# Kernel tuning notes

Measured on AMD Instinct MI355X. Metric: run time of the kernel, lower is better.

Reference implementation:

```python
import jax, jax.numpy as jnp
import numpy as np

B, VH, VL, EP = 4, 130, 120, 256
DIN, DEP, D, H, NL = 256, 128, 512, 16, 8
HID = 4 * D

def _pe(x, base=1000.0):
    # sinusoidal positional encoding (base=1000 as in the module)
    L, Dm = x.shape[-2], x.shape[-1]
    pos = jnp.arange(L, dtype=jnp.float32)
    ch = jnp.arange(Dm, dtype=jnp.float32)
    ang = pos[:, None] / (base ** (2.0 * ch / ch[-1]))[None]
    enc = jnp.where(ch % 2 == 0, jnp.sin(ang), jnp.cos(ang))
    return x + enc

def _ln(x, g, b):
    m = x.mean(-1, keepdims=True)
    v = ((x - m) ** 2).mean(-1, keepdims=True)
    return (x - m) / jnp.sqrt(v + 1e-5) * g + b

def _gmha(x, rots, trans, mask_bias, qkv_w, out_w, out_b, g, b, r_s, d_s):
    # ESM3 geometric multi-head attention (algorithm 6)
    xn = _ln(x, g, b)
    qkv = (xn @ qkv_w.T).reshape(x.shape[0], x.shape[1], 5, H, 3)  # [B,L,5,H,3]
    qkv = jnp.einsum('brid,brfhd->brfhi', rots, qkv)               # rotate into global frame
    Qr, Kr, Qd, Kd, V = (qkv[..., f, :, :] for f in range(5))
    scale = 3.0 ** -0.5
    Ar = jnp.einsum('bihd,bjhd->bijh', Qr, Kr) * jax.nn.softplus(r_s) * scale
    qd = Qd + trans[:, :, None, :]
    kd = Kd + trans[:, :, None, :]
    dist = jnp.linalg.norm(qd[:, :, None] - kd[:, None], axis=-1)  # [B,i,j,H]
    logits = Ar - dist * jax.nn.softplus(d_s) * scale + mask_bias[..., None]
    A = jax.nn.softmax(logits, axis=2)
    o = jnp.einsum('bijh,bjhd->bihd', A, V)
    o = jnp.einsum('brji,brhj->brhi', rots, o)                     # rotate back (R^T)
    return o.reshape(x.shape[0], x.shape[1], H * 3) @ out_w.T + out_b

def _swiglu(x, g, b, w12, w3):
    # SwiGLU transition (dropout is identity in eval)
    h = _ln(x, g, b) @ w12.T
    a, v = jnp.split(h, 2, axis=-1)
    return (jax.nn.silu(a) * v) @ w3.T

def _forward(vh_x, vl_x, vh_rots, vh_trans, vl_rots, vl_trans, ep_feats, ep_rots, ep_trans,
             vh_emb_w, vl_emb_w, tgt_emb_w, qkv_w, out_w, out_b, ln_g, ln_b, r_scale, d_scale,
             ln2_g, ln2_b, w12, w3, out_vh_w, out_vh_gate_w, out_vh_gate_b,
             out_vl_w, out_vl_gate_w, out_vl_gate_b, vh_mask, vl_mask, ep_mask):
    emb = jnp.concatenate([_pe(vh_x @ vh_emb_w.T), _pe(vl_x @ vl_emb_w.T), ep_feats @ tgt_emb_w.T], axis=1)
    rots = jnp.concatenate([vh_rots, vl_rots, ep_rots], axis=1)
    trans = jnp.concatenate([vh_trans, vl_trans, ep_trans], axis=1)
    mask = jnp.concatenate([vh_mask, vl_mask, ep_mask], axis=1)
    mask_bias = jnp.where(mask[:, :, None] | mask[:, None, :], -1e9, 0.0)
    for i in range(NL):
        emb = emb + _gmha(emb, rots, trans, mask_bias, qkv_w[i], out_w[i], out_b[i],
                          ln_g[i], ln_b[i], r_scale[i], d_scale[i])
        emb = emb + _swiglu(emb, ln2_g[i], ln2_b[i], w12[i], w3[i])
    vh_e, vl_e = emb[:, :VH], emb[:, VH:VH + VL]
    vh_upd = (vh_e @ out_vh_w.T) * jax.nn.sigmoid(vh_e @ out_vh_gate_w.T + out_vh_gate_b)
    vl_upd = (vl_e @ out_vl_w.T) * jax.nn.sigmoid(vl_e @ out_vl_gate_w.T + out_vl_gate_b)
    vh_out = jnp.where(~vh_mask[..., None], vh_x + vh_upd, vh_x)
    vl_out = jnp.where(~vl_mask[..., None], vl_x + vl_upd, vl_x)
    return vh_out, vl_out

def setup_inputs():
    key = jax.random.key(0)
    ks = iter(jax.random.split(key, 40))
    s = 0.02
    return dict(
        vh_x=jax.random.normal(next(ks), (B, VH, DIN)),
        vl_x=jax.random.normal(next(ks), (B, VL, DIN)),
        vh_rots=jax.random.normal(next(ks), (B, VH, 3, 3)),
        vh_trans=jax.random.normal(next(ks), (B, VH, 3)),
        vl_rots=jax.random.normal(next(ks), (B, VL, 3, 3)),
        vl_trans=jax.random.normal(next(ks), (B, VL, 3)),
        ep_feats=jax.random.normal(next(ks), (B, EP, DEP)),
        ep_rots=jax.random.normal(next(ks), (B, EP, 3, 3)),
        ep_trans=jax.random.normal(next(ks), (B, EP, 3)),
        vh_mask=jnp.zeros((B, VH), dtype=bool),
        vl_mask=jnp.zeros((B, VL), dtype=bool),
        ep_mask=jax.random.randint(next(ks), (B, EP), 0, 2).astype(bool),
        vh_emb_w=jax.random.normal(next(ks), (D, DIN)) * s,
        vl_emb_w=jax.random.normal(next(ks), (D, DIN)) * s,
        tgt_emb_w=jax.random.normal(next(ks), (D, DEP)) * s,
        qkv_w=jax.random.normal(next(ks), (NL, H * 15, D)) * s,
        out_w=jax.random.normal(next(ks), (NL, D, H * 3)) * s,
        out_b=jnp.zeros((NL, D)),
        ln_g=jnp.ones((NL, D)), ln_b=jnp.zeros((NL, D)),
        r_scale=jnp.zeros((NL, H)), d_scale=jnp.zeros((NL, H)),
        ln2_g=jnp.ones((NL, D)), ln2_b=jnp.zeros((NL, D)),
        w12=jax.random.normal(next(ks), (NL, 2 * HID, D)) * s,
        w3=jax.random.normal(next(ks), (NL, D, HID)) * s,
        out_vh_w=jax.random.normal(next(ks), (DIN, D)) * s,
        out_vh_gate_w=jax.random.normal(next(ks), (DIN, D)) * s,
        out_vh_gate_b=jnp.full((DIN,), -2.0),
        out_vl_w=jax.random.normal(next(ks), (DIN, D)) * s,
        out_vl_gate_w=jax.random.normal(next(ks), (DIN, D)) * s,
        out_vl_gate_b=jnp.full((DIN,), -2.0),
    )

def reference(vh_x, vl_x, vh_rots, vh_trans, vl_rots, vl_trans, ep_feats, ep_rots, ep_trans,
              vh_mask, vl_mask, ep_mask,
              vh_emb_w, vl_emb_w, tgt_emb_w, qkv_w, out_w, out_b, ln_g, ln_b, r_scale, d_scale,
              ln2_g, ln2_b, w12, w3, out_vh_w, out_vh_gate_w, out_vh_gate_b,
              out_vl_w, out_vl_gate_w, out_vl_gate_b):
    return _forward(vh_x, vl_x, vh_rots, vh_trans, vl_rots, vl_trans, ep_feats, ep_rots, ep_trans,
                    vh_emb_w, vl_emb_w, tgt_emb_w, qkv_w, out_w, out_b, ln_g, ln_b, r_scale, d_scale,
                    ln2_g, ln2_b, w12, w3, out_vh_w, out_vh_gate_w, out_vh_gate_b,
                    out_vl_w, out_vl_gate_w, out_vl_gate_b, vh_mask, vl_mask, ep_mask)
```

## Files before the change

### kernel.cpp

```cpp
#include <hip/hip_runtime.h>
#include <hip/hip_bf16.h>
#include <math.h>
#include <stdint.h>

#define B_ 4
#define VH_ 130
#define VL_ 120
#define EP_ 256
#define R_ 506
#define RP_ 512
#define DIN_ 256
#define DEP_ 128
#define D_ 512
#define H_ 16
#define NL_ 8
#define HID_ 2048

#define MODE_STORE 0
#define MODE_ADD_BIAS 1

typedef _Float16 half8 __attribute__((ext_vector_type(8)));
typedef float f32x4 __attribute__((ext_vector_type(4)));

#define ASYNC16(ldsdst, gsrc)                                                  \
  __builtin_amdgcn_global_load_lds(                                            \
      (const __attribute__((address_space(1))) unsigned int*)(gsrc),           \
      (__attribute__((address_space(3))) unsigned int*)(ldsdst), 16, 0, 0)

__global__ __launch_bounds__(256) void gemm16_kernel(
    const _Float16* __restrict__ A, const _Float16* __restrict__ W,
    float* __restrict__ C, const float* __restrict__ bias,
    int M, int N, int K, int mode) {
  __shared__ _Float16 Al[4][4096];
  __shared__ _Float16 Bl[4][2048];

  const int t = threadIdx.x;
  const int nbm = (M + 127) >> 7;
  const int nwg = gridDim.x;
  int bid = blockIdx.x;
  if ((nwg & 7) == 0) {
    int q = nwg >> 3;
    bid = (bid & 7) * q + (bid >> 3);
  }
  const int bm = bid % nbm, bn = bid / nbm;
  const int lane = t & 63;
  const int w = t >> 6;
  const int wm = w >> 1, wn = w & 1;

  const int r0 = t >> 2;
  const int cp = t & 3;
  const int gc = cp ^ ((r0 >> 1) & 3);
  int gr0 = bm * 128 + r0;       if (gr0 >= M) gr0 = M - 1;
  int gr1 = bm * 128 + 64 + r0;  if (gr1 >= M) gr1 = M - 1;
  int gcol = bn * 64 + r0;       if (gcol >= N) gcol = N - 1;
  const _Float16* pA0 = A + (size_t)gr0 * K + gc * 8;
  const _Float16* pA1 = A + (size_t)gr1 * K + gc * 8;
  const _Float16* pB  = W + (size_t)gcol * K + gc * 8;

#define STAGE(buf, kt)                                                         \
  do {                                                                         \
    ASYNC16(&Al[buf][t * 8], pA0 + (size_t)(kt) * 32);                         \
    ASYNC16(&Al[buf][2048 + t * 8], pA1 + (size_t)(kt) * 32);                  \
    ASYNC16(&Bl[buf][t * 8], pB + (size_t)(kt) * 32);                          \
  } while (0)

  f32x4 acc[4][2];
#pragma unroll
  for (int i = 0; i < 4; i++)
#pragma unroll
    for (int j = 0; j < 2; j++) acc[i][j] = (f32x4){0.f, 0.f, 0.f, 0.f};

  const int nt = K >> 5;
  STAGE(0, 0); STAGE(1, 1); STAGE(2, 2);

  const int rl = lane & 15;
  const int ca = (lane >> 4) ^ ((rl >> 1) & 3);
  for (int kt = 0; kt < nt; ++kt) {
    if (kt < nt - 2)       asm volatile("s_waitcnt vmcnt(6)" ::: "memory");
    else if (kt == nt - 2) asm volatile("s_waitcnt vmcnt(3)" ::: "memory");
    else                   asm volatile("s_waitcnt vmcnt(0)" ::: "memory");
    __builtin_amdgcn_s_barrier();
    const int buf = kt & 3;
    const _Float16* Ab = &Al[buf][(wm * 64 + rl) * 32 + ca * 8];
    const _Float16* Bb = &Bl[buf][(wn * 32 + rl) * 32 + ca * 8];
    half8 af[4], bf[2];
#pragma unroll
    for (int i = 0; i < 4; i++) af[i] = *(const half8*)(Ab + i * 512);
#pragma unroll
    for (int j = 0; j < 2; j++) bf[j] = *(const half8*)(Bb + j * 512);
#pragma unroll
    for (int i = 0; i < 4; i++)
#pragma unroll
      for (int j = 0; j < 2; j++)
        acc[i][j] = __builtin_amdgcn_mfma_f32_16x16x32_f16(af[i], bf[j],
                                                           acc[i][j], 0, 0, 0);
    if (kt + 3 < nt) STAGE((kt + 3) & 3, kt + 3);
  }
#undef STAGE

  const int rb = bm * 128 + wm * 64 + ((lane >> 4) << 2);
  const int cb = bn * 64 + wn * 32 + (lane & 15);
#pragma unroll
  for (int i = 0; i < 4; i++) {
#pragma unroll
    for (int j = 0; j < 2; j++) {
      int col = cb + j * 16;
      if (col >= N) continue;
#pragma unroll
      for (int q = 0; q < 4; q++) {
        int row = rb + i * 16 + q;
        if (row >= M) continue;
        size_t idx = (size_t)row * N + col;
        float v = acc[i][j][q];
        if (mode == MODE_STORE) C[idx] = v;
        else {
          float bb = bias ? bias[col] : 0.f;
          C[idx] = C[idx] + v + bb;
        }
      }
    }
  }
}

__global__ __launch_bounds__(256) void gemm16sw_kernel(
    const _Float16* __restrict__ A, const _Float16* __restrict__ Wa,
    const _Float16* __restrict__ Wv, _Float16* __restrict__ Gh,
    int M, int K) {
  __shared__ _Float16 Al[4][4096];
  __shared__ _Float16 Ba[4][2048];
  __shared__ _Float16 Bv[4][2048];

  const int t = threadIdx.x;
  const int nbm = (M + 127) >> 7;
  const int nwg = gridDim.x;
  int bid = blockIdx.x;
  if ((nwg & 7) == 0) {
    int q = nwg >> 3;
    bid = (bid & 7) * q + (bid >> 3);
// ... 73 lines not shown
#pragma unroll
    for (int j = 0; j < 2; j++) {
      int col = cb + j * 16;
#pragma unroll
      for (int q = 0; q < 4; q++) {
        int row = rb + i * 16 + q;
        if (row >= M) continue;
        float a = aca[i][j][q];
        float v = acv[i][j][q];
        Gh[(size_t)row * HID_ + col] = (_Float16)((a / (1.f + expf(-a))) * v);
      }
    }
  }
}

__global__ __launch_bounds__(256) void gemm_kernel(
    const float* __restrict__ A, const float* __restrict__ W,
    float* __restrict__ C, const float* __restrict__ bias,
    int M, int N, int K,
    int A_rpb, int A_R, int A_base,
    int C_rpb, int C_R, int C_base,
    int mode) {
  __shared__ __align__(16) float As[16][68];
  __shared__ __align__(16) float Bs[16][68];

  const int t = threadIdx.x;
  const int bm = blockIdx.y, bn = blockIdx.x;
  const int ty = t >> 4, tx = t & 15;
  const int lr = t >> 2;
  const int c0 = (t & 3) * 4;

  const int ma = bm * 64 + lr;
  const bool va = (ma < M);
  int ar = 0;
  if (va) ar = (ma / A_rpb) * A_R + A_base + (ma % A_rpb);
  const float* pA = A + (size_t)ar * K + c0;

  const int nw = bn * 64 + lr;
  const bool vw = (nw < N);
  const float* pW = W + (size_t)nw * K + c0;

  float acc[4][4];
#pragma unroll
  for (int i = 0; i < 4; i++)
#pragma unroll
    for (int j = 0; j < 4; j++) acc[i][j] = 0.f;

  for (int k0 = 0; k0 < K; k0 += 16) {
    __syncthreads();
    float4 avv = va ? *(const float4*)(pA + k0) : make_float4(0.f, 0.f, 0.f, 0.f);
    float4 wvv = vw ? *(const float4*)(pW + k0) : make_float4(0.f, 0.f, 0.f, 0.f);
    As[c0 + 0][lr] = avv.x; As[c0 + 1][lr] = avv.y;
    As[c0 + 2][lr] = avv.z; As[c0 + 3][lr] = avv.w;
    Bs[c0 + 0][lr] = wvv.x; Bs[c0 + 1][lr] = wvv.y;
    Bs[c0 + 2][lr] = wvv.z; Bs[c0 + 3][lr] = wvv.w;
    __syncthreads();
#pragma unroll
    for (int kk = 0; kk < 16; kk++) {
      float4 a = *(const float4*)&As[kk][ty * 4];
      float4 bv = *(const float4*)&Bs[kk][tx * 4];
      float av[4] = {a.x, a.y, a.z, a.w};
      float bb[4] = {bv.x, bv.y, bv.z, bv.w};
#pragma unroll
      for (int i = 0; i < 4; i++)
#pragma unroll
        for (int j = 0; j < 4; j++) acc[i][j] += av[i] * bb[j];
    }
  }

  const int m0 = bm * 64 + ty * 4;
  const int n0 = bn * 64 + tx * 4;
#pragma unroll
  for (int i = 0; i < 4; i++) {
    int m = m0 + i;
    if (m >= M) continue;
    int crow = (m / C_rpb) * C_R + C_base + (m % C_rpb);
    float* cp = C + (size_t)crow * N;
#pragma unroll
    for (int j = 0; j < 4; j++) {
      int n = n0 + j;
      if (n >= N) continue;
      float r = acc[i][j];
      if (mode == MODE_STORE) cp[n] = r;
      else { float bb = bias ? bias[n] : 0.f; cp[n] = cp[n] + r + bb; }
    }
  }
}

__global__ __launch_bounds__(256) void ln_kernel(
    const float* __restrict__ x, const float* __restrict__ g,
    const float* __restrict__ b, _Float16* __restrict__ out) {
  const int row = blockIdx.x;
  const int t = threadIdx.x;
  const float* xr = x + (size_t)row * D_;
  float v0 = xr[t], v1 = xr[t + 256];
  float s = v0 + v1, s2 = v0 * v0 + v1 * v1;
#pragma unroll
  for (int o = 32; o > 0; o >>= 1) {
    s += __shfl_down(s, o);
// ... 6 lines not shown
  if (t == 0) {
    float ss = w1[0] + w1[1] + w1[2] + w1[3];
    float ss2 = w2[0] + w2[1] + w2[2] + w2[3];
    float mean = ss * (1.f / D_);
    float var = ss2 * (1.f / D_) - mean * mean;
    mv[0] = mean;
    mv[1] = rsqrtf(var + 1e-5f);
  }
  __syncthreads();
  float mean = mv[0], inv = mv[1];
  _Float16* orow = out + (size_t)row * D_;
  orow[t] = (_Float16)((v0 - mean) * inv * g[t] + b[t]);
  orow[t + 256] = (_Float16)((v1 - mean) * inv * g[t + 256] + b[t + 256]);
}

__global__ void tohalf_kernel(const float* __restrict__ src,
                              _Float16* __restrict__ dst, int n8) {
  for (int i = blockIdx.x * blockDim.x + threadIdx.x; i < n8;
       i += gridDim.x * blockDim.x) {
    const float4* s = (const float4*)(src + (size_t)i * 8);
    float4 x = s[0], y = s[1];
    half8 h = {(_Float16)x.x, (_Float16)x.y, (_Float16)x.z, (_Float16)x.w,
               (_Float16)y.x, (_Float16)y.y, (_Float16)y.z, (_Float16)y.w};
    *(half8*)(dst + (size_t)i * 8) = h;
  }
}

__global__ void concat_kernel(
    const float* __restrict__ vh_rots, const float* __restrict__ vh_trans,
    const float* __restrict__ vl_rots, const float* __restrict__ vl_trans,
    const float* __restrict__ ep_rots, const float* __restrict__ ep_trans,
    const int* __restrict__ vh_mask, const int* __restrict__ vl_mask,
    const int* __restrict__ ep_mask,
    float* __restrict__ rots, float* __restrict__ trans, int* __restrict__ mask) {
  int idx = blockIdx.x * blockDim.x + threadIdx.x;
  if (idx >= B_ * R_) return;
  int b = idx / R_, r = idx % R_;
  const float* sr; const float* st; int sm;
  if (r < VH_) {
    sr = vh_rots + (size_t)(b * VH_ + r) * 9;
    st = vh_trans + (size_t)(b * VH_ + r) * 3;
    sm = vh_mask[b * VH_ + r];
  } else if (r < VH_ + VL_) {
    int rr = r - VH_;
    sr = vl_rots + (size_t)(b * VL_ + rr) * 9;
    st = vl_trans + (size_t)(b * VL_ + rr) * 3;
    sm = vl_mask[b * VL_ + rr];
  } else {
    int rr = r - VH_ - VL_;
    sr = ep_rots + (size_t)(b * EP_ + rr) * 9;
    st = ep_trans + (size_t)(b * EP_ + rr) * 3;
    sm = ep_mask[b * EP_ + rr];
  }
#pragma unroll
  for (int k = 0; k < 9; k++) rots[(size_t)idx * 9 + k] = sr[k];
#pragma unroll
  for (int k = 0; k < 3; k++) trans[(size_t)idx * 3 + k] = st[k];
  mask[idx] = sm;
}

__global__ void pad_kernel(const int* __restrict__ mask_c, int* __restrict__ maskp,
                           float* __restrict__ Kt, float* __restrict__ PKt,
                           float* __restrict__ Vt) {
  int idx = blockIdx.x * blockDim.x + threadIdx.x;
  if (idx < B_ * RP_) {
    int b = idx >> 9, j = idx & (RP_ - 1);
    maskp[idx] = (j < R_) ? mask_c[b * R_ + j] : 1;
  } else if (idx < B_ * RP_ + 3 * B_ * H_ * 3 * (RP_ - R_)) {
    int p = idx - B_ * RP_;
    int a = p / (B_ * H_ * 3 * (RP_ - R_));
    int q = p % (B_ * H_ * 3 * (RP_ - R_));
    int chan = q / (RP_ - R_), jj = q % (RP_ - R_);
    float* dst = (a == 0) ? Kt : (a == 1) ? PKt : Vt;
    dst[(size_t)chan * RP_ + R_ + jj] = 0.f;
  }
}

__global__ void pe_kernel(float* __restrict__ emb) {
  int idx = blockIdx.x * blockDim.x + threadIdx.x;
  const int total = B_ * (VH_ + VL_) * D_;
  if (idx >= total) return;
  int d = idx & (D_ - 1);
  int rb = idx >> 9;
  int r = rb % (VH_ + VL_);
  int b = rb / (VH_ + VL_);
  float pos = (r < VH_) ? (float)r : (float)(r - VH_);
  float ang = pos * expf((float)d * (-2.0f / 511.0f) * 6.907755278982137f);
  float enc = (d & 1) ? cosf(ang) : sinf(ang);
  emb[((size_t)b * R_ + r) * D_ + d] += enc;
}

__global__ __launch_bounds__(128) void rotate_kernel(
    const float* __restrict__ qkv_raw, const float* __restrict__ rots,
    const float* __restrict__ trans, float* __restrict__ Qrow,
    float* __restrict__ PQrow, float* __restrict__ Kt,
    float* __restrict__ PKt, float* __restrict__ Vt) {
  const int blk = blockIdx.x;
  const int b = blk / R_;
  const int r = blk % R_;
  const int t = threadIdx.x;
  __shared__ float Rm[9], tr[3], raw[240];
  if (t < 9) Rm[t] = rots[(size_t)blk * 9 + t];
  if (t >= 9 && t < 12) tr[t - 9] = trans[(size_t)blk * 3 + (t - 9)];
  for (int i = t; i < 240; i += 128) raw[i] = qkv_raw[(size_t)blk * 240 + i];
// ... 13 lines not shown
      dst[o] = r0; dst[o + 1] = r1; dst[o + 2] = r2;
    } else {
      float* dst = (f == 1) ? Kt : (f == 3) ? PKt : Vt;
      size_t base = ((size_t)(b * H_ + h) * 3) * RP_ + r;
      dst[base] = r0; dst[base + RP_] = r1; dst[base + 2 * RP_] = r2;
    }
  }
}

__global__ __launch_bounds__(256) void attn2_kernel(
    const float* __restrict__ Qrow, const float* __restrict__ PQrow,
    const float* __restrict__ Kt, const float* __restrict__ PKt,
    const float* __restrict__ Vt, const float* __restrict__ rots,
    const int* __restrict__ mask, const int* __restrict__ maskp,
    const float* __restrict__ rs, const float* __restrict__ ds,
    float* __restrict__ o) {
  const int blk = blockIdx.x;
  const int b = blk / (R_ / 2);
  const int ip = blk % (R_ / 2);
  const int i0 = ip * 2;
  const int t = threadIdx.x;
  const int lane = t & 63;
  const int w = t >> 6;

  __shared__ float qs[2][48], ps[2][48], og[2][48];
  __shared__ float crs[16], cds[16];
  __shared__ int mi[2];

  if (t < 96) {
    int io = t / 48, k2 = t % 48;
    int i = i0 + io;
// ... 62 lines not shown
      ox0 += p0 * vx; oy0 += p0 * vy; oz0 += p0 * vz;
      ox1 += p1 * vx; oy1 += p1 * vy; oz1 += p1 * vz;
    }
#pragma unroll
    for (int s = 1; s < 64; s <<= 1) {
      s0 += __shfl_xor(s0, s); s1 += __shfl_xor(s1, s);
      ox0 += __shfl_xor(ox0, s); oy0 += __shfl_xor(oy0, s); oz0 += __shfl_xor(oz0, s);
      ox1 += __shfl_xor(ox1, s); oy1 += __shfl_xor(oy1, s); oz1 += __shfl_xor(oz1, s);
    }
    if (lane == 0) {
      og[0][h * 3] = ox0 / s0; og[0][h * 3 + 1] = oy0 / s0; og[0][h * 3 + 2] = oz0 / s0;
      og[1][h * 3] = ox1 / s1; og[1][h * 3 + 1] = oy1 / s1; og[1][h * 3 + 2] = oz1 / s1;
    }
  }
  __syncthreads();
  if (t < 96) {
    int io = t / 48, idx = t % 48;
    int h = idx / 3, i3 = idx % 3;
    int i = i0 + io;
    const float* Rm = rots + ((size_t)(b * R_ + i)) * 9;
    float val = Rm[0 + i3] * og[io][h * 3 + 0] +
                Rm[3 + i3] * og[io][h * 3 + 1] +
                Rm[6 + i3] * og[io][h * 3 + 2];
    o[((size_t)(b * R_ + i)) * 48 + idx] = val;
  }
}

__global__ void combine_kernel(
    const float* __restrict__ x, const float* __restrict__ t1,
    const float* __restrict__ t2, const float* __restrict__ gate_b,
    const int* __restrict__ mask, float* __restrict__ out, int total) {
  int idx = blockIdx.x * blockDim.x + threadIdx.x;
  if (idx >= total) return;
  int dm = idx & (DIN_ - 1);
  int row = idx >> 8;
  float xv = x[idx];
  if (mask[row]) {
    out[idx] = xv;
  } else {
    float gate = 1.f / (1.f + expf(-(t2[idx] + gate_b[dm])));
    out[idx] = xv + t1[idx] * gate;
  }
}

extern "C" void kernel_launch(void* const* d_in, const int* in_sizes, int n_in,
                              void* d_out, int out_size, void* d_ws, size_t ws_size,
                              hipStream_t stream) {
  const float* vh_x = (const float*)d_in[0];
  const float* vl_x = (const float*)d_in[1];
  const float* vh_rots = (const float*)d_in[2];
  const float* vh_trans = (const float*)d_in[3];
  const float* vl_rots = (const float*)d_in[4];
  const float* vl_trans = (const float*)d_in[5];
  const float* ep_feats = (const float*)d_in[6];
  const float* ep_rots = (const float*)d_in[7];
  const float* ep_trans = (const float*)d_in[8];
// ... 22 lines not shown
  const float* out_vl_gate_b = (const float*)d_in[31];

  const int BR = B_ * R_;

  uint8_t* P = (uint8_t*)d_ws;
  auto alloc = [&](size_t bytes) {
    uint8_t* p = P;
    P += (bytes + 255) & ~(size_t)255;
    return p;
  };
  float* emb = (float*)alloc((size_t)BR * D_ * 4);
  _Float16* xnh = (_Float16*)alloc((size_t)BR * D_ * 2);
  float* qkvr = (float*)alloc((size_t)BR * 240 * 4);
  float* Qrow = (float*)alloc((size_t)BR * 48 * 4);
  float* PQrow = (float*)alloc((size_t)BR * 48 * 4);
  float* ob = (float*)alloc((size_t)BR * 48 * 4);
  float* Kt = (float*)alloc((size_t)B_ * H_ * 3 * RP_ * 4);
  float* PKt = (float*)alloc((size_t)B_ * H_ * 3 * RP_ * 4);
  float* Vt = (float*)alloc((size_t)B_ * H_ * 3 * RP_ * 4);
  _Float16* ghalf = (_Float16*)alloc((size_t)BR * HID_ * 2);
  float* rots_c = (float*)alloc((size_t)BR * 9 * 4);
  float* trans_c = (float*)alloc((size_t)BR * 3 * 4);
  int* mask_c = (int*)alloc((size_t)BR * 4);
  int* maskp = (int*)alloc((size_t)B_ * RP_ * 4);
  float* t1 = (float*)alloc((size_t)B_ * VH_ * DIN_ * 4);
  float* t2 = (float*)alloc((size_t)B_ * VH_ * DIN_ * 4);
  _Float16* qkvh = (_Float16*)alloc((size_t)NL_ * 240 * D_ * 2);
  _Float16* w12h = (_Float16*)alloc((size_t)NL_ * 2 * HID_ * D_ * 2);
  _Float16* w3h = (_Float16*)alloc((size_t)NL_ * D_ * HID_ * 2);

  auto gemm32 = [&](const float* A, const float* W, float* C, const float* bias,
                    int M, int N, int K, int Arpb, int AR, int Abase, int Crpb,
                    int CR, int Cbase, int mode) {
    dim3 g((N + 63) / 64, (M + 63) / 64);
    gemm_kernel<<<g, 256, 0, stream>>>(A, W, C, bias, M, N, K, Arpb, AR, Abase,
                                       Crpb, CR, Cbase, mode);
  };
  auto gemm16 = [&](const _Float16* A, const _Float16* W, float* C,
                    const float* bias, int M, int N, int K, int mode) {
    int nbm = (M + 127) / 128, nbn = (N + 63) / 64;
    gemm16_kernel<<<nbm * nbn, 256, 0, stream>>>(A, W, C, bias, M, N, K, mode);
  };

  {
    int n8q = NL_ * 240 * D_ / 8;
    int n8a = NL_ * 2 * HID_ * D_ / 8;
    int n8c = NL_ * D_ * HID_ / 8;
    tohalf_kernel<<<dim3(min((n8q + 255) / 256, 2048)), 256, 0, stream>>>(qkv_w, qkvh, n8q);
    tohalf_kernel<<<dim3(min((n8a + 255) / 256, 4096)), 256, 0, stream>>>(w12, w12h, n8a);
    tohalf_kernel<<<dim3(min((n8c + 255) / 256, 4096)), 256, 0, stream>>>(w3, w3h, n8c);
  }

  concat_kernel<<<(BR + 255) / 256, 256, 0, stream>>>(
      vh_rots, vh_trans, vl_rots, vl_trans, ep_rots, ep_trans, vh_mask,
      vl_mask, ep_mask, rots_c, trans_c, mask_c);
  {
    int total = B_ * RP_ + 3 * B_ * H_ * 3 * (RP_ - R_);
    pad_kernel<<<(total + 255) / 256, 256, 0, stream>>>(mask_c, maskp, Kt, PKt, Vt);
  }

  gemm32(vh_x, vh_emb_w, emb, nullptr, B_ * VH_, D_, DIN_, B_ * VH_, B_ * VH_, 0,
         VH_, R_, 0, MODE_STORE);
  gemm32(vl_x, vl_emb_w, emb, nullptr, B_ * VL_, D_, DIN_, B_ * VL_, B_ * VL_, 0,
         VL_, R_, VH_, MODE_STORE);
  gemm32(ep_feats, tgt_emb_w, emb, nullptr, B_ * EP_, D_, DEP_, B_ * EP_,
         B_ * EP_, 0, EP_, R_, VH_ + VL_, MODE_STORE);
  {
    int total = B_ * (VH_ + VL_) * D_;
    pe_kernel<<<(total + 255) / 256, 256, 0, stream>>>(emb);
  }

  for (int l = 0; l < NL_; l++) {
    const _Float16* qwh = qkvh + (size_t)l * 240 * D_;
    const float* ow = out_w + (size_t)l * D_ * 48;
    const float* obias = out_b + (size_t)l * D_;
    const float* lg = ln_g + (size_t)l * D_;
    const float* lb = ln_b + (size_t)l * D_;
    const float* l2g = ln2_g + (size_t)l * D_;
    const float* l2b = ln2_b + (size_t)l * D_;
    const float* rs = r_scale + (size_t)l * H_;
    const float* dsc = d_scale + (size_t)l * H_;
    const _Float16* w12ah = w12h + (size_t)l * 2 * HID_ * D_;
    const _Float16* w12bh = w12ah + (size_t)HID_ * D_;
    const _Float16* w3lh = w3h + (size_t)l * D_ * HID_;

    ln_kernel<<<BR, 256, 0, stream>>>(emb, lg, lb, xnh);
    gemm16(xnh, qwh, qkvr, nullptr, BR, 240, D_, MODE_STORE);
    rotate_kernel<<<BR, 128, 0, stream>>>(qkvr, rots_c, trans_c, Qrow, PQrow,
                                          Kt, PKt, Vt);
    attn2_kernel<<<B_ * (R_ / 2), 256, 0, stream>>>(Qrow, PQrow, Kt, PKt, Vt,
                                                    rots_c, mask_c, maskp, rs,
                                                    dsc, ob);
    gemm32(ob, ow, emb, obias, BR, D_, 48, BR, BR, 0, BR, BR, 0, MODE_ADD_BIAS);

    ln_kernel<<<BR, 256, 0, stream>>>(emb, l2g, l2b, xnh);
    {
      int nbm = (BR + 127) / 128, nbn = HID_ / 64;
      gemm16sw_kernel<<<nbm * nbn, 256, 0, stream>>>(xnh, w12ah, w12bh, ghalf,
                                                     BR, D_);
    }
    gemm16(ghalf, w3lh, emb, nullptr, BR, D_, HID_, MODE_ADD_BIAS);
  }

  gemm32(emb, out_vh_w, t1, nullptr, B_ * VH_, DIN_, D_, VH_, R_, 0, B_ * VH_,
         B_ * VH_, 0, MODE_STORE);
  gemm32(emb, out_vh_gate_w, t2, nullptr, B_ * VH_, DIN_, D_, VH_, R_, 0,
         B_ * VH_, B_ * VH_, 0, MODE_STORE);
  {
    int total = B_ * VH_ * DIN_;
    combine_kernel<<<(total + 255) / 256, 256, 0, stream>>>(
        vh_x, t1, t2, out_vh_gate_b, vh_mask, (float*)d_out, total);
  }
  gemm32(emb, out_vl_w, t1, nullptr, B_ * VL_, DIN_, D_, VL_, R_, VH_, B_ * VL_,
         B_ * VL_, 0, MODE_STORE);
  gemm32(emb, out_vl_gate_w, t2, nullptr, B_ * VL_, DIN_, D_, VL_, R_, VH_,
         B_ * VL_, B_ * VL_, 0, MODE_STORE);
  {
    int total = B_ * VL_ * DIN_;
    combine_kernel<<<(total + 255) / 256, 256, 0, stream>>>(
        vl_x, t1, t2, out_vl_gate_b, vl_mask,
        (float*)d_out + (size_t)B_ * VH_ * DIN_, total);
  }
}
```

Baseline: 1.324 ms.

## Replace fp32 GEMMs with fp16 MFMA, fuse PE, out-proj, gating, prep kernels

```diff
diff --git a/kernel.cpp b/kernel.cpp
--- a/kernel.cpp
+++ b/kernel.cpp
@@ -27,101 +27,6 @@
       (const __attribute__((address_space(1))) unsigned int*)(gsrc),           \
       (__attribute__((address_space(3))) unsigned int*)(ldsdst), 16, 0, 0)
 
-__global__ __launch_bounds__(256) void gemm16_kernel(
-    const _Float16* __restrict__ A, const _Float16* __restrict__ W,
-    float* __restrict__ C, const float* __restrict__ bias,
-    int M, int N, int K, int mode) {
-  __shared__ _Float16 Al[4][4096];
-  __shared__ _Float16 Bl[4][2048];
-
-  const int t = threadIdx.x;
-  const int nbm = (M + 127) >> 7;
-  const int nwg = gridDim.x;
-  int bid = blockIdx.x;
-  if ((nwg & 7) == 0) {
-    int q = nwg >> 3;
-    bid = (bid & 7) * q + (bid >> 3);
-  }
-  const int bm = bid % nbm, bn = bid / nbm;
-  const int lane = t & 63;
-  const int w = t >> 6;
-  const int wm = w >> 1, wn = w & 1;
-
-  const int r0 = t >> 2;
-  const int cp = t & 3;
-  const int gc = cp ^ ((r0 >> 1) & 3);
-  int gr0 = bm * 128 + r0;       if (gr0 >= M) gr0 = M - 1;
-  int gr1 = bm * 128 + 64 + r0;  if (gr1 >= M) gr1 = M - 1;
-  int gcol = bn * 64 + r0;       if (gcol >= N) gcol = N - 1;
-  const _Float16* pA0 = A + (size_t)gr0 * K + gc * 8;
-  const _Float16* pA1 = A + (size_t)gr1 * K + gc * 8;
-  const _Float16* pB  = W + (size_t)gcol * K + gc * 8;
-
-#define STAGE(buf, kt)                                                         \
-  do {                                                                         \
-    ASYNC16(&Al[buf][t * 8], pA0 + (size_t)(kt) * 32);                         \
-    ASYNC16(&Al[buf][2048 + t * 8], pA1 + (size_t)(kt) * 32);                  \
-    ASYNC16(&Bl[buf][t * 8], pB + (size_t)(kt) * 32);                          \
-  } while (0)
-
-  f32x4 acc[4][2];
-#pragma unroll
-  for (int i = 0; i < 4; i++)
-#pragma unroll
-    for (int j = 0; j < 2; j++) acc[i][j] = (f32x4){0.f, 0.f, 0.f, 0.f};
-
-  const int nt = K >> 5;
-  STAGE(0, 0); STAGE(1, 1); STAGE(2, 2);
-
-  const int rl = lane & 15;
-  const int ca = (lane >> 4) ^ ((rl >> 1) & 3);
-  for (int kt = 0; kt < nt; ++kt) {
-    if (kt < nt - 2)       asm volatile("s_waitcnt vmcnt(6)" ::: "memory");
-    else if (kt == nt - 2) asm volatile("s_waitcnt vmcnt(3)" ::: "memory");
-    else                   asm volatile("s_waitcnt vmcnt(0)" ::: "memory");
-    __builtin_amdgcn_s_barrier();
-    const int buf = kt & 3;
-    const _Float16* Ab = &Al[buf][(wm * 64 + rl) * 32 + ca * 8];
-    const _Float16* Bb = &Bl[buf][(wn * 32 + rl) * 32 + ca * 8];
-    half8 af[4], bf[2];
-#pragma unroll
-    for (int i = 0; i < 4; i++) af[i] = *(const half8*)(Ab + i * 512);
-#pragma unroll
-    for (int j = 0; j < 2; j++) bf[j] = *(const half8*)(Bb + j * 512);
-#pragma unroll
-    for (int i = 0; i < 4; i++)
-#pragma unroll
-      for (int j = 0; j < 2; j++)
-        acc[i][j] = __builtin_amdgcn_mfma_f32_16x16x32_f16(af[i], bf[j],
-                                                           acc[i][j], 0, 0, 0);
-    if (kt + 3 < nt) STAGE((kt + 3) & 3, kt + 3);
-  }
-#undef STAGE
-
-  const int rb = bm * 128 + wm * 64 + ((lane >> 4) << 2);
-  const int cb = bn * 64 + wn * 32 + (lane & 15);
-#pragma unroll
-  for (int i = 0; i < 4; i++) {
-#pragma unroll
-    for (int j = 0; j < 2; j++) {
-      int col = cb + j * 16;
-      if (col >= N) continue;
-#pragma unroll
-      for (int q = 0; q < 4; q++) {
-        int row = rb + i * 16 + q;
-        if (row >= M) continue;
-        size_t idx = (size_t)row * N + col;
-        float v = acc[i][j][q];
-        if (mode == MODE_STORE) C[idx] = v;
-        else {
-          float bb = bias ? bias[col] : 0.f;
-          C[idx] = C[idx] + v + bb;
-        }
-      }
-    }
-  }
-}
-
 __global__ __launch_bounds__(256) void gemm16sw_kernel(
     const _Float16* __restrict__ A, const _Float16* __restrict__ Wa,
     const _Float16* __restrict__ Wv, _Float16* __restrict__ Gh,
@@ -225,75 +130,208 @@
   }
 }
 
-__global__ __launch_bounds__(256) void gemm_kernel(
-    const float* __restrict__ A, const float* __restrict__ W,
+__global__ __launch_bounds__(256) void gemm16b_kernel(
+    const _Float16* __restrict__ A, const _Float16* __restrict__ W,
     float* __restrict__ C, const float* __restrict__ bias,
-    int M, int N, int K,
-    int A_rpb, int A_R, int A_base,
-    int C_rpb, int C_R, int C_base,
-    int mode) {
-  __shared__ __align__(16) float As[16][68];
-  __shared__ __align__(16) float Bs[16][68];
+    int M, int N, int K, int mode, int crpb, int cR, int cbase, int pe) {
+  __shared__ _Float16 Al[4][2048];
+  __shared__ _Float16 Bl[4][2048];
 
   const int t = threadIdx.x;
-  const int bm = blockIdx.y, bn = blockIdx.x;
-  const int ty = t >> 4, tx = t & 15;
-  const int lr = t >> 2;
-  const int c0 = (t & 3) * 4;
-
-  const int ma = bm * 64 + lr;
-  const bool va = (ma < M);
-  int ar = 0;
-  if (va) ar = (ma / A_rpb) * A_R + A_base + (ma % A_rpb);
-  const float* pA = A + (size_t)ar * K + c0;
-
-  const int nw = bn * 64 + lr;
-  const bool vw = (nw < N);
-  const float* pW = W + (size_t)nw * K + c0;
-
-  float acc[4][4];
-#pragma unroll
-  for (int i = 0; i < 4; i++)
-#pragma unroll
-    for (int j = 0; j < 4; j++) acc[i][j] = 0.f;
-
-  for (int k0 = 0; k0 < K; k0 += 16) {
-    __syncthreads();
-    float4 avv = va ? *(const float4*)(pA + k0) : make_float4(0.f, 0.f, 0.f, 0.f);
-    float4 wvv = vw ? *(const float4*)(pW + k0) : make_float4(0.f, 0.f, 0.f, 0.f);
-    As[c0 + 0][lr] = avv.x; As[c0 + 1][lr] = avv.y;
-    As[c0 + 2][lr] = avv.z; As[c0 + 3][lr] = avv.w;
-    Bs[c0 + 0][lr] = wvv.x; Bs[c0 + 1][lr] = wvv.y;
-    Bs[c0 + 2][lr] = wvv.z; Bs[c0 + 3][lr] = wvv.w;
-    __syncthreads();
-#pragma unroll
-    for (int kk = 0; kk < 16; kk++) {
-      float4 a = *(const float4*)&As[kk][ty * 4];
-      float4 bv = *(const float4*)&Bs[kk][tx * 4];
-      float av[4] = {a.x, a.y, a.z, a.w};
-      float bb[4] = {bv.x, bv.y, bv.z, bv.w};
-#pragma unroll
-      for (int i = 0; i < 4; i++)
-#pragma unroll
-        for (int j = 0; j < 4; j++) acc[i][j] += av[i] * bb[j];
-    }
-  }
-
-  const int m0 = bm * 64 + ty * 4;
-  const int n0 = bn * 64 + tx * 4;
-#pragma unroll
-  for (int i = 0; i < 4; i++) {
-    int m = m0 + i;
-    if (m >= M) continue;
-    int crow = (m / C_rpb) * C_R + C_base + (m % C_rpb);
-    float* cp = C + (size_t)crow * N;
-#pragma unroll
-    for (int j = 0; j < 4; j++) {
-      int n = n0 + j;
-      if (n >= N) continue;
-      float r = acc[i][j];
-      if (mode == MODE_STORE) cp[n] = r;
-      else { float bb = bias ? bias[n] : 0.f; cp[n] = cp[n] + r + bb; }
+  const int nbm = (M + 63) >> 6;
+  const int nwg = gridDim.x;
+  int bid = blockIdx.x;
+  if ((nwg & 7) == 0) {
+    int q = nwg >> 3;
+    bid = (bid & 7) * q + (bid >> 3);
+  }
+  const int bm = bid % nbm, bn = bid / nbm;
+  const int lane = t & 63;
+  const int w = t >> 6;
+  const int wm = w >> 1, wn = w & 1;
+
+  const int r0 = t >> 2;
+  const int cp = t & 3;
+  const int gc = cp ^ ((r0 >> 1) & 3);
+  int gr = bm * 64 + r0;    if (gr >= M) gr = M - 1;
+  int gcol = bn * 64 + r0;  if (gcol >= N) gcol = N - 1;
+  const _Float16* pA = A + (size_t)gr * K + gc * 8;
+  const _Float16* pB = W + (size_t)gcol * K + gc * 8;
+
+#define STAGE(buf, kt)                                                         \
+  do {                                                                         \
+    ASYNC16(&Al[buf][t * 8], pA + (size_t)(kt) * 32);                          \
+    ASYNC16(&Bl[buf][t * 8], pB + (size_t)(kt) * 32);                          \
+  } while (0)
+
+  f32x4 acc[2][2];
+#pragma unroll
+  for (int i = 0; i < 2; i++)
+#pragma unroll
+    for (int j = 0; j < 2; j++) acc[i][j] = (f32x4){0.f, 0.f, 0.f, 0.f};
+
+  const int nt = K >> 5;
+  STAGE(0, 0); STAGE(1, 1); STAGE(2, 2);
+
+  const int rl = lane & 15;
+  const int ca = (lane >> 4) ^ ((rl >> 1) & 3);
+  for (int kt = 0; kt < nt; ++kt) {
+    if (kt < nt - 2)       asm volatile("s_waitcnt vmcnt(4)" ::: "memory");
+    else if (kt == nt - 2) asm volatile("s_waitcnt vmcnt(2)" ::: "memory");
+    else                   asm volatile("s_waitcnt vmcnt(0)" ::: "memory");
+    __builtin_amdgcn_s_barrier();
+    const int buf = kt & 3;
+    half8 af[2], bf[2];
+#pragma unroll
+    for (int i = 0; i < 2; i++)
+      af[i] = *(const half8*)&Al[buf][(wm * 32 + i * 16 + rl) * 32 + ca * 8];
+#pragma unroll
+    for (int j = 0; j < 2; j++)
+      bf[j] = *(const half8*)&Bl[buf][(wn * 32 + j * 16 + rl) * 32 + ca * 8];
+#pragma unroll
+    for (int i = 0; i < 2; i++)
+#pragma unroll
+      for (int j = 0; j < 2; j++)
+        acc[i][j] = __builtin_amdgcn_mfma_f32_16x16x32_f16(af[i], bf[j],
+                                                           acc[i][j], 0, 0, 0);
+    if (kt + 3 < nt) STAGE((kt + 3) & 3, kt + 3);
+  }
+#undef STAGE
+
+  const float PEK = -0.02703623196464017f;
+  const int rb = bm * 64 + wm * 32 + ((lane >> 4) << 2);
+  const int cb = bn * 64 + wn * 32 + (lane & 15);
+#pragma unroll
+  for (int i = 0; i < 2; i++) {
+#pragma unroll
+    for (int j = 0; j < 2; j++) {
+      int col = cb + j * 16;
+      if (col >= N) continue;
+#pragma unroll
+      for (int q = 0; q < 4; q++) {
+        int row = rb + i * 16 + q;
+        if (row >= M) continue;
+        int crow = (row / crpb) * cR + cbase + row % crpb;
+        size_t idx = (size_t)crow * N + col;
+        float v = acc[i][j][q];
+        if (pe) {
+          float pos = (float)(row % crpb);
+          float ang = pos * expf((float)col * PEK);
+          v += (col & 1) ? cosf(ang) : sinf(ang);
+        }
+        if (mode == MODE_STORE) C[idx] = v;
+        else {
+          float bb = bias ? bias[col] : 0.f;
+          C[idx] = C[idx] + v + bb;
+        }
+      }
+    }
+  }
+}
+
+__global__ __launch_bounds__(256) void gemm16gate_kernel(
+    const _Float16* __restrict__ A, const _Float16* __restrict__ Wv,
+    const _Float16* __restrict__ Wg, const float* __restrict__ x,
+    const float* __restrict__ gb, const int* __restrict__ mask,
+    float* __restrict__ out, int M, int K, int arpb, int aR, int abase) {
+  __shared__ _Float16 Al[4][2048];
+  __shared__ _Float16 Bva[4][2048];
+  __shared__ _Float16 Bga[4][2048];
+
+  const int t = threadIdx.x;
+  const int nbm = (M + 63) >> 6;
+  const int nwg = gridDim.x;
+  int bid = blockIdx.x;
+  if ((nwg & 7) == 0) {
+    int q = nwg >> 3;
+    bid = (bid & 7) * q + (bid >> 3);
+  }
+  const int bm = bid % nbm, bn = bid / nbm;
+  const int lane = t & 63;
+  const int w = t >> 6;
+  const int wm = w >> 1, wn = w & 1;
+
+  const int r0 = t >> 2;
+  const int cp = t & 3;
+  const int gc = cp ^ ((r0 >> 1) & 3);
+  int gr = bm * 64 + r0;  if (gr >= M) gr = M - 1;
+  int ar = (gr / arpb) * aR + abase + gr % arpb;
+  const int gcol = bn * 64 + r0;
+  const _Float16* pA  = A + (size_t)ar * K + gc * 8;
+  const _Float16* pBv = Wv + (size_t)gcol * K + gc * 8;
+  const _Float16* pBg = Wg + (size_t)gcol * K + gc * 8;
+
+#define STAGE(buf, kt)                                                         \
+  do {                                                                         \
+    ASYNC16(&Al[buf][t * 8], pA + (size_t)(kt) * 32);                          \
+    ASYNC16(&Bva[buf][t * 8], pBv + (size_t)(kt) * 32);                        \
+    ASYNC16(&Bga[buf][t * 8], pBg + (size_t)(kt) * 32);                        \
+  } while (0)
+
+  f32x4 acv[2][2], acg[2][2];
+#pragma unroll
+  for (int i = 0; i < 2; i++)
+#pragma unroll
+    for (int j = 0; j < 2; j++) {
+      acv[i][j] = (f32x4){0.f, 0.f, 0.f, 0.f};
+      acg[i][j] = (f32x4){0.f, 0.f, 0.f, 0.f};
+    }
+
+  const int nt = K >> 5;
+  STAGE(0, 0); STAGE(1, 1); STAGE(2, 2);
+
+  const int rl = lane & 15;
+  const int ca = (lane >> 4) ^ ((rl >> 1) & 3);
+  for (int kt = 0; kt < nt; ++kt) {
+    if (kt < nt - 2)       asm volatile("s_waitcnt vmcnt(6)" ::: "memory");
+    else if (kt == nt - 2) asm volatile("s_waitcnt vmcnt(3)" ::: "memory");
+    else                   asm volatile("s_waitcnt vmcnt(0)" ::: "memory");
+    __builtin_amdgcn_s_barrier();
+    const int buf = kt & 3;
+    half8 af[2], bv[2], bg2[2];
+#pragma unroll
+    for (int i = 0; i < 2; i++)
+      af[i] = *(const half8*)&Al[buf][(wm * 32 + i * 16 + rl) * 32 + ca * 8];
+#pragma unroll
+    for (int j = 0; j < 2; j++) {
+      bv[j] = *(const half8*)&Bva[buf][(wn * 32 + j * 16 + rl) * 32 + ca * 8];
+      bg2[j] = *(const half8*)&Bga[buf][(wn * 32 + j * 16 + rl) * 32 + ca * 8];
+    }
+#pragma unroll
+    for (int i = 0; i < 2; i++)
+#pragma unroll
+      for (int j = 0; j < 2; j++) {
+        acv[i][j] = __builtin_amdgcn_mfma_f32_16x16x32_f16(af[i], bv[j],
+                                                           acv[i][j], 0, 0, 0);
+        acg[i][j] = __builtin_amdgcn_mfma_f32_16x16x32_f16(af[i], bg2[j],
+                                                           acg[i][j], 0, 0, 0);
+      }
+    if (kt + 3 < nt) STAGE((kt + 3) & 3, kt + 3);
+  }
+#undef STAGE
+
+  const int rb = bm * 64 + wm * 32 + ((lane >> 4) << 2);
+  const int cb = bn * 64 + wn * 32 + (lane & 15);
+#pragma unroll
+  for (int i = 0; i < 2; i++) {
+#pragma unroll
+    for (int j = 0; j < 2; j++) {
+      int col = cb + j * 16;
+#pragma unroll
+      for (int q = 0; q < 4; q++) {
+        int row = rb + i * 16 + q;
+        if (row >= M) continue;
+        size_t idx = (size_t)row * DIN_ + col;
+        float xv = x[idx];
+        float res;
+        if (mask[row]) {
+          res = xv;
+        } else {
+          float gate = 1.f / (1.f + expf(-(acg[i][j][q] + gb[col])));
+          res = xv + acv[i][j][q] * gate;
+        }
+        out[idx] = res;
+      }
     }
   }
 }
@@ -330,6 +368,26 @@
   orow[t + 256] = (_Float16)((v1 - mean) * inv * g[t + 256] + b[t + 256]);
 }
 
+struct ThSegs {
+  const float* src[13];
+  _Float16* dst[13];
+  int cum[14];
+};
+__global__ void tohalf_multi_kernel(ThSegs sg) {
+  int total = sg.cum[13];
+  for (int i = blockIdx.x * blockDim.x + threadIdx.x; i < total;
+       i += gridDim.x * blockDim.x) {
+    int s = 0;
+    while (i >= sg.cum[s + 1]) s++;
+    int off = i - sg.cum[s];
+    const float4* p = (const float4*)(sg.src[s] + (size_t)off * 8);
+    float4 x = p[0], y = p[1];
+    half8 h = {(_Float16)x.x, (_Float16)x.y, (_Float16)x.z, (_Float16)x.w,
+               (_Float16)y.x, (_Float16)y.y, (_Float16)y.z, (_Float16)y.w};
+    *(half8*)(sg.dst[s] + (size_t)off * 8) = h;
+  }
+}
+
 __global__ void tohalf_kernel(const float* __restrict__ src,
                               _Float16* __restrict__ dst, int n8) {
   for (int i = blockIdx.x * blockDim.x + threadIdx.x; i < n8;
@@ -342,68 +400,55 @@
   }
 }
 
-__global__ void concat_kernel(
+__global__ void prep_kernel(
     const float* __restrict__ vh_rots, const float* __restrict__ vh_trans,
     const float* __restrict__ vl_rots, const float* __restrict__ vl_trans,
     const float* __restrict__ ep_rots, const float* __restrict__ ep_trans,
     const int* __restrict__ vh_mask, const int* __restrict__ vl_mask,
-    const int* __restrict__ ep_mask,
-    float* __restrict__ rots, float* __restrict__ trans, int* __restrict__ mask) {
-  int idx = blockIdx.x * blockDim.x + threadIdx.x;
-  if (idx >= B_ * R_) return;
-  int b = idx / R_, r = idx % R_;
-  const float* sr; const float* st; int sm;
-  if (r < VH_) {
-    sr = vh_rots + (size_t)(b * VH_ + r) * 9;
-    st = vh_trans + (size_t)(b * VH_ + r) * 3;
-    sm = vh_mask[b * VH_ + r];
-  } else if (r < VH_ + VL_) {
-    int rr = r - VH_;
-    sr = vl_rots + (size_t)(b * VL_ + rr) * 9;
-    st = vl_trans + (size_t)(b * VL_ + rr) * 3;
-    sm = vl_mask[b * VL_ + rr];
-  } else {
-    int rr = r - VH_ - VL_;
-    sr = ep_rots + (size_t)(b * EP_ + rr) * 9;
-    st = ep_trans + (size_t)(b * EP_ + rr) * 3;
-    sm = ep_mask[b * EP_ + rr];
-  }
-#pragma unroll
-  for (int k = 0; k < 9; k++) rots[(size_t)idx * 9 + k] = sr[k];
-#pragma unroll
-  for (int k = 0; k < 3; k++) trans[(size_t)idx * 3 + k] = st[k];
-  mask[idx] = sm;
-}
-
-__global__ void pad_kernel(const int* __restrict__ mask_c, int* __restrict__ maskp,
-                           float* __restrict__ Kt, float* __restrict__ PKt,
-                           float* __restrict__ Vt) {
+    const int* __restrict__ ep_mask, float* __restrict__ rots,
+    float* __restrict__ trans, int* __restrict__ mask,
+    int* __restrict__ maskp, float* __restrict__ Kt, float* __restrict__ PKt,
+    float* __restrict__ Vt) {
   int idx = blockIdx.x * blockDim.x + threadIdx.x;
   if (idx < B_ * RP_) {
-    int b = idx >> 9, j = idx & (RP_ - 1);
-    maskp[idx] = (j < R_) ? mask_c[b * R_ + j] : 1;
-  } else if (idx < B_ * RP_ + 3 * B_ * H_ * 3 * (RP_ - R_)) {
+    int b = idx >> 9, r = idx & (RP_ - 1);
+    if (r >= R_) {
+      maskp[idx] = 1;
+      return;
+    }
+    const float* sr; const float* st; int sm;
+    if (r < VH_) {
+      sr = vh_rots + (size_t)(b * VH_ + r) * 9;
+      st = vh_trans + (size_t)(b * VH_ + r) * 3;
+      sm = vh_mask[b * VH_ + r];
+    } else if (r < VH_ + VL_) {
+      int rr = r - VH_;
+      sr = vl_rots + (size_t)(b * VL_ + rr) * 9;
+      st = vl_trans + (size_t)(b * VL_ + rr) * 3;
+      sm = vl_mask[b * VL_ + rr];
+    } else {
+      int rr = r - VH_ - VL_;
+      sr = ep_rots + (size_t)(b * EP_ + rr) * 9;
+      st = ep_trans + (size_t)(b * EP_ + rr) * 3;
+      sm = ep_mask[b * EP_ + rr];
+    }
+    int lin = b * R_ + r;
+    maskp[idx] = sm;
+    mask[lin] = sm;
+#pragma unroll
+    for (int k = 0; k < 9; k++) rots[(size_t)lin * 9 + k] = sr[k];
+#pragma unroll
+    for (int k = 0; k < 3; k++) trans[(size_t)lin * 3 + k] = st[k];
+  } else {
     int p = idx - B_ * RP_;
-    int a = p / (B_ * H_ * 3 * (RP_ - R_));
-    int q = p % (B_ * H_ * 3 * (RP_ - R_));
+    const int per = B_ * H_ * 3 * (RP_ - R_);
+    if (p >= 3 * per) return;
+    int a = p / per;
+    int q = p % per;
     int chan = q / (RP_ - R_), jj = q % (RP_ - R_);
     float* dst = (a == 0) ? Kt : (a == 1) ? PKt : Vt;
     dst[(size_t)chan * RP_ + R_ + jj] = 0.f;
   }
-}
-
-__global__ void pe_kernel(float* __restrict__ emb) {
-  int idx = blockIdx.x * blockDim.x + threadIdx.x;
-  const int total = B_ * (VH_ + VL_) * D_;
-  if (idx >= total) return;
-  int d = idx & (D_ - 1);
-  int rb = idx >> 9;
-  int r = rb % (VH_ + VL_);
-  int b = rb / (VH_ + VL_);
-  float pos = (r < VH_) ? (float)r : (float)(r - VH_);
-  float ang = pos * expf((float)d * (-2.0f / 511.0f) * 6.907755278982137f);
-  float enc = (d & 1) ? cosf(ang) : sinf(ang);
-  emb[((size_t)b * R_ + r) * D_ + d] += enc;
 }
 
 __global__ __launch_bounds__(128) void rotate_kernel(
@@ -447,7 +492,8 @@
     const float* __restrict__ Vt, const float* __restrict__ rots,
     const int* __restrict__ mask, const int* __restrict__ maskp,
     const float* __restrict__ rs, const float* __restrict__ ds,
-    float* __restrict__ o) {
+    const float* __restrict__ out_w, const float* __restrict__ out_b,
+    float* __restrict__ emb) {
   const int blk = blockIdx.x;
   const int b = blk / (R_ / 2);
   const int ip = blk % (R_ / 2);
@@ -540,32 +586,31 @@
     }
   }
   __syncthreads();
-  if (t < 96) {
-    int io = t / 48, idx = t % 48;
-    int h = idx / 3, i3 = idx % 3;
-    int i = i0 + io;
-    const float* Rm = rots + ((size_t)(b * R_ + i)) * 9;
-    float val = Rm[0 + i3] * og[io][h * 3 + 0] +
-                Rm[3 + i3] * og[io][h * 3 + 1] +
-                Rm[6 + i3] * og[io][h * 3 + 2];
-    o[((size_t)(b * R_ + i)) * 48 + idx] = val;
-  }
-}
-
-__global__ void combine_kernel(
-    const float* __restrict__ x, const float* __restrict__ t1,
-    const float* __restrict__ t2, const float* __restrict__ gate_b,
-    const int* __restrict__ mask, float* __restrict__ out, int total) {
-  int idx = blockIdx.x * blockDim.x + threadIdx.x;
-  if (idx >= total) return;
-  int dm = idx & (DIN_ - 1);
-  int row = idx >> 8;
-  float xv = x[idx];
-  if (mask[row]) {
-    out[idx] = xv;
-  } else {
-    float gate = 1.f / (1.f + expf(-(t2[idx] + gate_b[dm])));
-    out[idx] = xv + t1[idx] * gate;
+  float r0v0 = 0.f, r0v1 = 0.f;
+  if (t < 48) {
+    int h = t / 3, i3 = t % 3;
+    const float* Rm0 = rots + ((size_t)(b * R_ + i0)) * 9;
+    const float* Rm1 = rots + ((size_t)(b * R_ + i0 + 1)) * 9;
+    r0v0 = Rm0[0 + i3] * og[0][h * 3 + 0] + Rm0[3 + i3] * og[0][h * 3 + 1] +
+           Rm0[6 + i3] * og[0][h * 3 + 2];
+    r0v1 = Rm1[0 + i3] * og[1][h * 3 + 0] + Rm1[3 + i3] * og[1][h * 3 + 1] +
+           Rm1[6 + i3] * og[1][h * 3 + 2];
+  }
+  __syncthreads();
+  if (t < 48) { og[0][t] = r0v0; og[1][t] = r0v1; }
+  __syncthreads();
+#pragma unroll
+  for (int io = 0; io < 2; io++) {
+    float* erow = emb + ((size_t)(b * R_ + i0 + io)) * D_;
+#pragma unroll
+    for (int half = 0; half < 2; half++) {
+      int c = half * 256 + t;
+      const float* wr = out_w + (size_t)c * 48;
+      float s = out_b[c];
+#pragma unroll
+      for (int k = 0; k < 48; k++) s += og[io][k] * wr[k];
+      erow[c] += s;
+    }
   }
 }
 
@@ -618,7 +663,6 @@
   float* qkvr = (float*)alloc((size_t)BR * 240 * 4);
   float* Qrow = (float*)alloc((size_t)BR * 48 * 4);
   float* PQrow = (float*)alloc((size_t)BR * 48 * 4);
-  float* ob = (float*)alloc((size_t)BR * 48 * 4);
   float* Kt = (float*)alloc((size_t)B_ * H_ * 3 * RP_ * 4);
   float* PKt = (float*)alloc((size_t)B_ * H_ * 3 * RP_ * 4);
   float* Vt = (float*)alloc((size_t)B_ * H_ * 3 * RP_ * 4);
@@ -627,52 +671,63 @@
   float* trans_c = (float*)alloc((size_t)BR * 3 * 4);
   int* mask_c = (int*)alloc((size_t)BR * 4);
   int* maskp = (int*)alloc((size_t)B_ * RP_ * 4);
-  float* t1 = (float*)alloc((size_t)B_ * VH_ * DIN_ * 4);
-  float* t2 = (float*)alloc((size_t)B_ * VH_ * DIN_ * 4);
+  _Float16* embh = (_Float16*)alloc((size_t)BR * D_ * 2);
   _Float16* qkvh = (_Float16*)alloc((size_t)NL_ * 240 * D_ * 2);
   _Float16* w12h = (_Float16*)alloc((size_t)NL_ * 2 * HID_ * D_ * 2);
   _Float16* w3h = (_Float16*)alloc((size_t)NL_ * D_ * HID_ * 2);
-
-  auto gemm32 = [&](const float* A, const float* W, float* C, const float* bias,
-                    int M, int N, int K, int Arpb, int AR, int Abase, int Crpb,
-                    int CR, int Cbase, int mode) {
-    dim3 g((N + 63) / 64, (M + 63) / 64);
-    gemm_kernel<<<g, 256, 0, stream>>>(A, W, C, bias, M, N, K, Arpb, AR, Abase,
-                                       Crpb, CR, Cbase, mode);
-  };
-  auto gemm16 = [&](const _Float16* A, const _Float16* W, float* C,
-                    const float* bias, int M, int N, int K, int mode) {
-    int nbm = (M + 127) / 128, nbn = (N + 63) / 64;
-    gemm16_kernel<<<nbm * nbn, 256, 0, stream>>>(A, W, C, bias, M, N, K, mode);
-  };
+  _Float16* vhxh = (_Float16*)alloc((size_t)B_ * VH_ * DIN_ * 2);
+  _Float16* vlxh = (_Float16*)alloc((size_t)B_ * VL_ * DIN_ * 2);
+  _Float16* eph = (_Float16*)alloc((size_t)B_ * EP_ * DEP_ * 2);
+  _Float16* vhewh = (_Float16*)alloc((size_t)D_ * DIN_ * 2);
+  _Float16* vlewh = (_Float16*)alloc((size_t)D_ * DIN_ * 2);
+  _Float16* tgewh = (_Float16*)alloc((size_t)D_ * DEP_ * 2);
+  _Float16* ovhw = (_Float16*)alloc((size_t)DIN_ * D_ * 2);
+  _Float16* ovhgw = (_Float16*)alloc((size_t)DIN_ * D_ * 2);
+  _Float16* ovlw = (_Float16*)alloc((size_t)DIN_ * D_ * 2);
+  _Float16* ovlgw = (_Float16*)alloc((size_t)DIN_ * D_ * 2);
 
   {
-    int n8q = NL_ * 240 * D_ / 8;
-    int n8a = NL_ * 2 * HID_ * D_ / 8;
-    int n8c = NL_ * D_ * HID_ / 8;
-    tohalf_kernel<<<dim3(min((n8q + 255) / 256, 2048)), 256, 0, stream>>>(qkv_w, qkvh, n8q);
-    tohalf_kernel<<<dim3(min((n8a + 255) / 256, 4096)), 256, 0, stream>>>(w12, w12h, n8a);
-    tohalf_kernel<<<dim3(min((n8c + 255) / 256, 4096)), 256, 0, stream>>>(w3, w3h, n8c);
-  }
-
-  concat_kernel<<<(BR + 255) / 256, 256, 0, stream>>>(
-      vh_rots, vh_trans, vl_rots, vl_trans, ep_rots, ep_trans, vh_mask,
-      vl_mask, ep_mask, rots_c, trans_c, mask_c);
+    ThSegs sg;
+    const float* srcs[13] = {qkv_w, w12, w3, vh_x, vl_x, ep_feats,
+                             vh_emb_w, vl_emb_w, tgt_emb_w,
+                             out_vh_w, out_vh_gate_w, out_vl_w, out_vl_gate_w};
+    _Float16* dsts[13] = {qkvh, w12h, w3h, vhxh, vlxh, eph,
+                          vhewh, vlewh, tgewh, ovhw, ovhgw, ovlw, ovlgw};
+    int n8s[13] = {NL_ * 240 * D_ / 8, NL_ * 2 * HID_ * D_ / 8,
+                   NL_ * D_ * HID_ / 8, B_ * VH_ * DIN_ / 8,
+                   B_ * VL_ * DIN_ / 8, B_ * EP_ * DEP_ / 8,
+                   D_ * DIN_ / 8, D_ * DIN_ / 8, D_ * DEP_ / 8,
+                   DIN_ * D_ / 8, DIN_ * D_ / 8, DIN_ * D_ / 8, DIN_ * D_ / 8};
+    int c = 0;
+    for (int i = 0; i < 13; i++) {
+      sg.src[i] = srcs[i]; sg.dst[i] = dsts[i];
+      sg.cum[i] = c; c += n8s[i];
+    }
+    sg.cum[13] = c;
+    tohalf_multi_kernel<<<2048, 256, 0, stream>>>(sg);
+  }
+
   {
     int total = B_ * RP_ + 3 * B_ * H_ * 3 * (RP_ - R_);
-    pad_kernel<<<(total + 255) / 256, 256, 0, stream>>>(mask_c, maskp, Kt, PKt, Vt);
-  }
-
-  gemm32(vh_x, vh_emb_w, emb, nullptr, B_ * VH_, D_, DIN_, B_ * VH_, B_ * VH_, 0,
-         VH_, R_, 0, MODE_STORE);
-  gemm32(vl_x, vl_emb_w, emb, nullptr, B_ * VL_, D_, DIN_, B_ * VL_, B_ * VL_, 0,
-         VL_, R_, VH_, MODE_STORE);
-  gemm32(ep_feats, tgt_emb_w, emb, nullptr, B_ * EP_, D_, DEP_, B_ * EP_,
-         B_ * EP_, 0, EP_, R_, VH_ + VL_, MODE_STORE);
-  {
-    int total = B_ * (VH_ + VL_) * D_;
-    pe_kernel<<<(total + 255) / 256, 256, 0, stream>>>(emb);
-  }
+    prep_kernel<<<(total + 255) / 256, 256, 0, stream>>>(
+        vh_rots, vh_trans, vl_rots, vl_trans, ep_rots, ep_trans, vh_mask,
+        vl_mask, ep_mask, rots_c, trans_c, mask_c, maskp, Kt, PKt, Vt);
+  }
+
+  auto gemm16b = [&](const _Float16* A, const _Float16* W, float* C,
+                     const float* bias, int M, int N, int K, int mode,
+                     int crpb, int cR, int cbase, int pe) {
+    int nbm = (M + 63) / 64, nbn = (N + 63) / 64;
+    gemm16b_kernel<<<nbm * nbn, 256, 0, stream>>>(A, W, C, bias, M, N, K, mode,
+                                                  crpb, cR, cbase, pe);
+  };
+
+  gemm16b(vhxh, vhewh, emb, nullptr, B_ * VH_, D_, DIN_, MODE_STORE,
+          VH_, R_, 0, 1);
+  gemm16b(vlxh, vlewh, emb, nullptr, B_ * VL_, D_, DIN_, MODE_STORE,
+          VL_, R_, VH_, 1);
+  gemm16b(eph, tgewh, emb, nullptr, B_ * EP_, D_, DEP_, MODE_STORE,
+          EP_, R_, VH_ + VL_, 0);
 
   for (int l = 0; l < NL_; l++) {
     const _Float16* qwh = qkvh + (size_t)l * 240 * D_;
@@ -689,13 +744,12 @@
     const _Float16* w3lh = w3h + (size_t)l * D_ * HID_;
 
     ln_kernel<<<BR, 256, 0, stream>>>(emb, lg, lb, xnh);
-    gemm16(xnh, qwh, qkvr, nullptr, BR, 240, D_, MODE_STORE);
+    gemm16b(xnh, qwh, qkvr, nullptr, BR, 240, D_, MODE_STORE, BR, BR, 0, 0);
     rotate_kernel<<<BR, 128, 0, stream>>>(qkvr, rots_c, trans_c, Qrow, PQrow,
                                           Kt, PKt, Vt);
-    attn2_kernel<<<B_ * (R_ / 2), 256, 0, stream>>>(Qrow, PQrow, Kt, PKt, Vt,
-                                                    rots_c, mask_c, maskp, rs,
-                                                    dsc, ob);
-    gemm32(ob, ow, emb, obias, BR, D_, 48, BR, BR, 0, BR, BR, 0, MODE_ADD_BIAS);
+    attn2_kernel<<<B_ * (R_ / 2), 256, 0, stream>>>(
+        Qrow, PQrow, Kt, PKt, Vt, rots_c, mask_c, maskp, rs, dsc, ow, obias,
+        emb);
 
     ln_kernel<<<BR, 256, 0, stream>>>(emb, l2g, l2b, xnh);
     {
@@ -703,26 +757,23 @@
       gemm16sw_kernel<<<nbm * nbn, 256, 0, stream>>>(xnh, w12ah, w12bh, ghalf,
                                                      BR, D_);
     }
-    gemm16(ghalf, w3lh, emb, nullptr, BR, D_, HID_, MODE_ADD_BIAS);
-  }
-
-  gemm32(emb, out_vh_w, t1, nullptr, B_ * VH_, DIN_, D_, VH_, R_, 0, B_ * VH_,
-         B_ * VH_, 0, MODE_STORE);
-  gemm32(emb, out_vh_gate_w, t2, nullptr, B_ * VH_, DIN_, D_, VH_, R_, 0,
-         B_ * VH_, B_ * VH_, 0, MODE_STORE);
+    gemm16b(ghalf, w3lh, emb, nullptr, BR, D_, HID_, MODE_ADD_BIAS,
+            BR, BR, 0, 0);
+  }
+
+  tohalf_kernel<<<1024, 256, 0, stream>>>(emb, embh, BR * D_ / 8);
   {
-    int total = B_ * VH_ * DIN_;
-    combine_kernel<<<(total + 255) / 256, 256, 0, stream>>>(
-        vh_x, t1, t2, out_vh_gate_b, vh_mask, (float*)d_out, total);
-  }
-  gemm32(emb, out_vl_w, t1, nullptr, B_ * VL_, DIN_, D_, VL_, R_, VH_, B_ * VL_,
-         B_ * VL_, 0, MODE_STORE);
-  gemm32(emb, out_vl_gate_w, t2, nullptr, B_ * VL_, DIN_, D_, VL_, R_, VH_,
-         B_ * VL_, B_ * VL_, 0, MODE_STORE);
+    int M = B_ * VH_;
+    int nbm = (M + 63) / 64;
+    gemm16gate_kernel<<<nbm * 4, 256, 0, stream>>>(
+        embh, ovhw, ovhgw, vh_x, out_vh_gate_b, vh_mask, (float*)d_out, M, D_,
+        VH_, R_, 0);
+  }
   {
-    int total = B_ * VL_ * DIN_;
-    combine_kernel<<<(total + 255) / 256, 256, 0, stream>>>(
-        vl_x, t1, t2, out_vl_gate_b, vl_mask,
-        (float*)d_out + (size_t)B_ * VH_ * DIN_, total);
-  }
-}
+    int M = B_ * VL_;
+    int nbm = (M + 63) / 64;
+    gemm16gate_kernel<<<nbm * 4, 256, 0, stream>>>(
+        embh, ovlw, ovlgw, vl_x, out_vl_gate_b, vl_mask,
+        (float*)d_out + (size_t)B_ * VH_ * DIN_, M, D_, VL_, R_, VH_);
+  }
+}
```

After: 1.312 ms. No clear change (-0.9%).
